# Kernel optimization log

Measured on AMD Instinct MI355X. Metric: run time of the kernel, lower is better.

## Reference

```python
import jax, jax.numpy as jnp
import numpy as np

N_NODES = 100000
N_EDGES = 3200000
F_IN = 16


def gcn_conv(x, edge_index, W, b):
    """PyG GCNConv: x' = D^{-1/2} (A + I) D^{-1/2} (x W) + b,
    with degree computed after adding self-loops."""
    n = x.shape[0]
    xw = x @ W  # [N, F_out]
    row, col = edge_index[0], edge_index[1]  # messages flow row -> col
    ones = jnp.ones(row.shape, dtype=x.dtype)
    deg = jax.ops.segment_sum(ones, col, num_segments=n) + 1.0  # +1 for self-loop
    dinv = jax.lax.rsqrt(deg)  # [N]
    norm = dinv[row] * dinv[col]  # [E]
    msg = xw[row] * norm[:, None]  # [E, F_out]
    out = jax.ops.segment_sum(msg, col, num_segments=n)
    out = out + xw * (1.0 / deg)[:, None]  # self-loop term: norm = 1/deg
    return out + b


def setup_inputs() -> dict:
    key = jax.random.key(0)
    ks = jax.random.split(key, 8)
    x = jax.random.normal(ks[0], (N_NODES, F_IN), dtype=jnp.float32)
    edge_index = jax.random.randint(ks[1], (2, N_EDGES), 0, N_NODES, dtype=jnp.int32)
    # GCNConv weights (glorot in PyG; random normal scaled for the reference)
    W1 = jax.random.normal(ks[2], (F_IN, 4), dtype=jnp.float32) * 0.3
    W2 = jax.random.normal(ks[3], (4, 2), dtype=jnp.float32) * 0.5
    W3 = jax.random.normal(ks[4], (2, 1), dtype=jnp.float32) * 0.7
    b1 = jnp.zeros((4,), jnp.float32)
    b2 = jnp.zeros((2,), jnp.float32)
    b3 = jnp.zeros((1,), jnp.float32)
    return {"x": x, "edge_index": edge_index, "W1": W1, "b1": b1,
            "W2": W2, "b2": b2, "W3": W3, "b3": b3}


def reference(x, edge_index, W1, b1, W2, b2, W3, b3):
    # encode(): GCNConv -> relu -> GCNConv -> relu -> GCNConv -> tanh
    # (dropout is identity in eval mode)
    h = jax.nn.relu(gcn_conv(x, edge_index, W1, b1))
    h = jax.nn.relu(gcn_conv(h, edge_index, W2, b2))
    return jnp.tanh(gcn_conv(h, edge_index, W3, b3))  # [N, 1]
```

## Files before the change

kernel.cpp:

```cpp
#include <hip/hip_runtime.h>
#include <math.h>


static constexpr int BLK    = 256;
static constexpr int BSHIFT = 7;
static constexpr int BCOLS  = 128;
static constexpr int CAP    = 5120;
static constexpr int PAD    = 16;
static constexpr int PBLK   = 512;
static constexpr int PITER  = 25;
static constexpr int SBLK   = 512;
static constexpr int GBLK   = 512;

__global__ void zero_cnt_kernel(int* __restrict__ cnt, int len) {
    int i = blockIdx.x * blockDim.x + threadIdx.x;
    if (i < len) cnt[i] = 0;
}

__global__ __launch_bounds__(PBLK) void partition_kernel(
        const int* __restrict__ row, const int* __restrict__ col,
        int* __restrict__ cnt, unsigned int* __restrict__ part,
        int e, int nbuck) {
    __shared__ int hist[1024];
    for (int j = threadIdx.x; j < nbuck; j += PBLK) hist[j] = 0;
    __syncthreads();

    const int base = blockIdx.x * (PBLK * PITER) + (int)threadIdx.x;
    unsigned int pay[PITER];
    unsigned int meta[PITER];
#pragma unroll
    for (int i = 0; i < PITER; ++i) {
        int idx = base + i * PBLK;
        bool ok = idx < e;
        int c = ok ? col[idx] : 0;
        int r = ok ? row[idx] : 0;
        int bk = c >> BSHIFT;
        pay[i] = ((unsigned int)(c & (BCOLS - 1)) << 17) | (unsigned int)r;
        if (ok) {
            int rnk = atomicAdd(&hist[bk], 1);
            meta[i] = ((unsigned int)bk << 18) | (unsigned int)rnk;
        } else {
            meta[i] = 0xFFFFFFFFu;
        }
    }
    __syncthreads();

    for (int j = threadIdx.x; j < nbuck; j += PBLK) {
        int h = hist[j];
        hist[j] = h ? atomicAdd(&cnt[j * PAD], h) : 0;
    }
    __syncthreads();

#pragma unroll
    for (int i = 0; i < PITER; ++i) {
        if (meta[i] != 0xFFFFFFFFu) {
            int bk  = (int)(meta[i] >> 18);
            int rnk = (int)(meta[i] & 0x3FFFFu);
            int off = hist[bk] + rnk;
            if (off < CAP)
                part[(size_t)bk * CAP + off] = pay[i];
        }
    }
}

__global__ __launch_bounds__(SBLK) void sort_y1_kernel(
        unsigned int* __restrict__ part, const int* __restrict__ cnt,
        const float* __restrict__ x, const float* __restrict__ W1,
        int* __restrict__ rs, int* __restrict__ re, float* __restrict__ dinv,
        float* __restrict__ y1, int n) {
    __shared__ unsigned int staged[CAP];
    __shared__ unsigned short srank[CAP];
    __shared__ int hist[BCOLS];
    __shared__ int scanb[BCOLS];
    const int b = blockIdx.x;
    const int m = min(cnt[b * PAD], CAP);
    const size_t segbase = (size_t)b * CAP;

    if (threadIdx.x < BCOLS) hist[threadIdx.x] = 0;
    __syncthreads();
    for (int k = threadIdx.x; k < m; k += SBLK) {
        unsigned int v = part[segbase + k];
        staged[k] = v;
        srank[k] = (unsigned short)atomicAdd(&hist[v >> 17], 1);
    }
    __syncthreads();

    if (threadIdx.x < BCOLS) scanb[threadIdx.x] = hist[threadIdx.x];
    __syncthreads();
    for (int off = 1; off < BCOLS; off <<= 1) {
        int v = 0;
        if (threadIdx.x < BCOLS && (int)threadIdx.x >= off)
            v = scanb[threadIdx.x - off];
        __syncthreads();
        if (threadIdx.x < BCOLS) scanb[threadIdx.x] += v;
        __syncthreads();
    }

    for (int k = threadIdx.x; k < m; k += SBLK) {
        unsigned int v = staged[k];
        int lc = (int)(v >> 17);
        int pos = (scanb[lc] - hist[lc]) + (int)srank[k];
        part[segbase + pos] = v & 0x1FFFFu;
    }

    int lc = (int)threadIdx.x >> 2;
    int f  = (int)threadIdx.x & 3;
    int node = b * BCOLS + lc;
    if (node < n) {
        int deg = hist[lc];
        float di = rsqrtf((float)(deg + 1));
        if (f == 0) {
            int start = (int)segbase + (scanb[lc] - deg);
            rs[node] = start;
            re[node] = start + deg;
            dinv[node] = di;
        }
        const float4* x4 = (const float4*)x + (size_t)node * 4;
        float4 r0 = x4[0], r1 = x4[1], r2 = x4[2], r3 = x4[3];
        float a = 0.0f;
        a = fmaf(r0.x, W1[0 * 4 + f], a);  a = fmaf(r0.y, W1[1 * 4 + f], a);
        a = fmaf(r0.z, W1[2 * 4 + f], a);  a = fmaf(r0.w, W1[3 * 4 + f], a);
        a = fmaf(r1.x, W1[4 * 4 + f], a);  a = fmaf(r1.y, W1[5 * 4 + f], a);
        a = fmaf(r1.z, W1[6 * 4 + f], a);  a = fmaf(r1.w, W1[7 * 4 + f], a);
        a = fmaf(r2.x, W1[8 * 4 + f], a);  a = fmaf(r2.y, W1[9 * 4 + f], a);
        a = fmaf(r2.z, W1[10 * 4 + f], a); a = fmaf(r2.w, W1[11 * 4 + f], a);
        a = fmaf(r3.x, W1[12 * 4 + f], a); a = fmaf(r3.y, W1[13 * 4 + f], a);
        a = fmaf(r3.z, W1[14 * 4 + f], a); a = fmaf(r3.w, W1[15 * 4 + f], a);
        y1[node * 4 + f] = a * di;
    }
}

template <int F, int FN, int ACT, int SUBW>
__global__ __launch_bounds__(GBLK) void gather_kernel(
        const int* __restrict__ rs, const int* __restrict__ re,
        const unsigned int* __restrict__ csr,
        const float* __restrict__ y, const float* __restrict__ dinv,
        const float* __restrict__ bias, const float* __restrict__ Wn,
        float* __restrict__ outv, int n) {
    int t = blockIdx.x * GBLK + (int)threadIdx.x;
    int node = t / SUBW;
    int lane = t % SUBW;
    if (node >= n) return;
    int s = rs[node], tend = re[node];
    float acc[F];
#pragma unroll
    for (int f = 0; f < F; ++f) acc[f] = 0.0f;
    const float4* y4 = (const float4*)y;
    const float2* y2p = (const float2*)y;
    for (int k = s + lane; k < tend; k += SUBW) {
        int r = (int)csr[k];
        if constexpr (F == 4) {
            float4 a = y4[r];
            acc[0] += a.x; acc[1] += a.y; acc[2] += a.z; acc[3] += a.w;
        } else if constexpr (F == 2) {
            float2 a = y2p[r];
            acc[0] += a.x; acc[1] += a.y;
        } else {
            acc[0] += y[r];
        }
    }
#pragma unroll
    for (int off = SUBW / 2; off > 0; off >>= 1)
#pragma unroll
        for (int f = 0; f < F; ++f) acc[f] += __shfl_xor(acc[f], off);
    if (lane == 0) {
        float di = dinv[node];
        float h[F];
#pragma unroll
        for (int f = 0; f < F; ++f) {
            float z = di * (acc[f] + y[node * F + f]) + bias[f];
            if (ACT == 1) z = fmaxf(z, 0.0f);
            if (ACT == 2) z = tanhf(z);
            h[f] = z;
        }
        if constexpr (FN > 0) {
            float o[FN];
#pragma unroll
            for (int g = 0; g < FN; ++g) o[g] = 0.0f;
#pragma unroll
            for (int f = 0; f < F; ++f)
#pragma unroll
                for (int g = 0; g < FN; ++g)
                    o[g] = fmaf(h[f], Wn[f * FN + g], o[g]);
#pragma unroll
            for (int g = 0; g < FN; ++g) outv[node * FN + g] = o[g] * di;
        } else {
#pragma unroll
            for (int f = 0; f < F; ++f) outv[node * F + f] = h[f];
        }
    }
}

extern "C" void kernel_launch(void* const* d_in, const int* in_sizes, int n_in,
                              void* d_out, int out_size, void* d_ws, size_t ws_size,
                              hipStream_t stream) {
    const float* x  = (const float*)d_in[0];
    const int*   ei = (const int*)d_in[1];
    const float* W1 = (const float*)d_in[2];
    const float* b1 = (const float*)d_in[3];
    const float* W2 = (const float*)d_in[4];
    const float* b2 = (const float*)d_in[5];
    const float* W3 = (const float*)d_in[6];
    const float* b3 = (const float*)d_in[7];
    float* out = (float*)d_out;

    const int n = in_sizes[0] / 16;
    const int e = in_sizes[1] / 2;
    const int* row = ei;
    const int* col = ei + e;

    const int nbuck = (n + BCOLS - 1) / BCOLS;

    size_t off = 0;
    auto take = [&](size_t cnt_) {
        char* p = (char*)d_ws + off * 4;
        off += (cnt_ + 15) & ~(size_t)15;
        return p;
    };
    int* cnt           = (int*)take((size_t)nbuck * PAD);
    unsigned int* part = (unsigned int*)take((size_t)nbuck * CAP);
    int* rs            = (int*)take(n);
    int* re            = (int*)take(n);
    float* dinv        = (float*)take(n);
    float* y1          = (float*)take(4 * n);
    float* y2          = (float*)take(2 * n);
    float* y3          = (float*)take(n);

    zero_cnt_kernel<<<(nbuck * PAD + BLK - 1) / BLK, BLK, 0, stream>>>(cnt, nbuck * PAD);

    const int pnb = (e + PBLK * PITER - 1) / (PBLK * PITER);
    partition_kernel<<<pnb, PBLK, 0, stream>>>(row, col, cnt, part, e, nbuck);

    sort_y1_kernel<<<nbuck, SBLK, 0, stream>>>(part, cnt, x, W1, rs, re, dinv, y1, n);

    constexpr int SUBW = 8;
    const int gg = (n * SUBW + GBLK - 1) / GBLK;

    gather_kernel<4, 2, 1, SUBW><<<gg, GBLK, 0, stream>>>(rs, re, part, y1, dinv, b1, W2, y2, n);
    gather_kernel<2, 1, 1, SUBW><<<gg, GBLK, 0, stream>>>(rs, re, part, y2, dinv, b2, W3, y3, n);
    gather_kernel<1, 0, 2, SUBW><<<gg, GBLK, 0, stream>>>(rs, re, part, y3, dinv, b3, nullptr, out, n);
}
```

Baseline: 121.8 us.

## Stage partition and sort scatters in shared memory for coalesced global writes

The partition kernel now sorts each block's edges by bucket in shared memory (via a block-wide exclusive scan over bucket counts), then writes them out contiguously so runs of edges for the same bucket land in consecutive global addresses. PITER is halved to fit the staging buffers in LDS, doubling the block count. The sort kernel similarly writes the locally sorted segment to an LDS buffer first and then copies it to global memory linearly. The aim is to replace scattered global writes with coalesced ones, at the cost of extra LDS traffic, more barriers, and lower occupancy from larger shared memory use.

New measurement: 113.3 us. 6.9% less time.

```diff
diff --git a/kernel.cpp b/kernel.cpp
--- a/kernel.cpp
+++ b/kernel.cpp
@@ -5,10 +5,12 @@
 static constexpr int BLK    = 256;
 static constexpr int BSHIFT = 7;
 static constexpr int BCOLS  = 128;
+static constexpr int NBMAX  = 1024;
 static constexpr int CAP    = 5120;
 static constexpr int PAD    = 16;
 static constexpr int PBLK   = 512;
-static constexpr int PITER  = 25;
+static constexpr int PITER  = 13;
+static constexpr int PCHUNK = PBLK * PITER;
 static constexpr int SBLK   = 512;
 static constexpr int GBLK   = 512;
 
@@ -21,45 +23,68 @@
         const int* __restrict__ row, const int* __restrict__ col,
         int* __restrict__ cnt, unsigned int* __restrict__ part,
         int e, int nbuck) {
-    __shared__ int hist[1024];
-    for (int j = threadIdx.x; j < nbuck; j += PBLK) hist[j] = 0;
-    __syncthreads();
-
-    const int base = blockIdx.x * (PBLK * PITER) + (int)threadIdx.x;
+    __shared__ unsigned int   staged[PCHUNK];
+    __shared__ unsigned short bkid[PCHUNK];
+    __shared__ int hist[NBMAX];
+    __shared__ int excl[NBMAX];
+    __shared__ int gbase[NBMAX];
+    __shared__ int sh[PBLK];
+    const int t = (int)threadIdx.x;
+    for (int j = t; j < NBMAX; j += PBLK) hist[j] = 0;
+    __syncthreads();
+
+    const int blockstart = blockIdx.x * PCHUNK;
+    const int m = min(PCHUNK, e - blockstart);
+
     unsigned int pay[PITER];
-    unsigned int meta[PITER];
+    int bks[PITER], rnk[PITER];
 #pragma unroll
     for (int i = 0; i < PITER; ++i) {
-        int idx = base + i * PBLK;
-        bool ok = idx < e;
-        int c = ok ? col[idx] : 0;
-        int r = ok ? row[idx] : 0;
-        int bk = c >> BSHIFT;
-        pay[i] = ((unsigned int)(c & (BCOLS - 1)) << 17) | (unsigned int)r;
-        if (ok) {
-            int rnk = atomicAdd(&hist[bk], 1);
-            meta[i] = ((unsigned int)bk << 18) | (unsigned int)rnk;
+        int idx = blockstart + i * PBLK + t;
+        if (idx < e) {
+            int c = col[idx], r = row[idx];
+            bks[i] = c >> BSHIFT;
+            pay[i] = ((unsigned int)(c & (BCOLS - 1)) << 17) | (unsigned int)r;
+            rnk[i] = atomicAdd(&hist[bks[i]], 1);
         } else {
-            meta[i] = 0xFFFFFFFFu;
-        }
-    }
-    __syncthreads();
-
-    for (int j = threadIdx.x; j < nbuck; j += PBLK) {
+            bks[i] = -1;
+        }
+    }
+    __syncthreads();
+
+    int a0 = hist[2 * t], a1 = hist[2 * t + 1];
+    sh[t] = a0 + a1;
+    __syncthreads();
+    for (int off = 1; off < PBLK; off <<= 1) {
+        int v = (t >= off) ? sh[t - off] : 0;
+        __syncthreads();
+        sh[t] += v;
+        __syncthreads();
+    }
+    int pairExcl = sh[t] - (a0 + a1);
+    excl[2 * t]     = pairExcl;
+    excl[2 * t + 1] = pairExcl + a0;
+    for (int j = t; j < nbuck; j += PBLK) {
         int h = hist[j];
-        hist[j] = h ? atomicAdd(&cnt[j * PAD], h) : 0;
+        gbase[j] = h ? atomicAdd(&cnt[j * PAD], h) : 0;
     }
     __syncthreads();
 
 #pragma unroll
     for (int i = 0; i < PITER; ++i) {
-        if (meta[i] != 0xFFFFFFFFu) {
-            int bk  = (int)(meta[i] >> 18);
-            int rnk = (int)(meta[i] & 0x3FFFFu);
-            int off = hist[bk] + rnk;
-            if (off < CAP)
-                part[(size_t)bk * CAP + off] = pay[i];
-        }
+        if (bks[i] >= 0) {
+            int pos = excl[bks[i]] + rnk[i];
+            staged[pos] = pay[i];
+            bkid[pos]   = (unsigned short)bks[i];
+        }
+    }
+    __syncthreads();
+
+    for (int k = t; k < m; k += PBLK) {
+        int bk  = bkid[k];
+        int off2 = gbase[bk] + (k - excl[bk]);
+        if (off2 < CAP)
+            part[(size_t)bk * CAP + off2] = staged[k];
     }
 }
 
@@ -68,7 +93,8 @@
         const float* __restrict__ x, const float* __restrict__ W1,
         int* __restrict__ rs, int* __restrict__ re, float* __restrict__ dinv,
         float* __restrict__ y1, int n) {
-    __shared__ unsigned int staged[CAP];
+    __shared__ unsigned int   staged[CAP];
+    __shared__ unsigned int   sorted[CAP];
     __shared__ unsigned short srank[CAP];
     __shared__ int hist[BCOLS];
     __shared__ int scanb[BCOLS];
@@ -99,9 +125,12 @@
     for (int k = threadIdx.x; k < m; k += SBLK) {
         unsigned int v = staged[k];
         int lc = (int)(v >> 17);
-        int pos = (scanb[lc] - hist[lc]) + (int)srank[k];
-        part[segbase + pos] = v & 0x1FFFFu;
-    }
+        sorted[(scanb[lc] - hist[lc]) + (int)srank[k]] = v & 0x1FFFFu;
+    }
+    __syncthreads();
+
+    for (int k = threadIdx.x; k < m; k += SBLK)
+        part[segbase + k] = sorted[k];
 
     int lc = (int)threadIdx.x >> 2;
     int f  = (int)threadIdx.x & 3;
@@ -228,7 +257,7 @@
 
     zero_cnt_kernel<<<(nbuck * PAD + BLK - 1) / BLK, BLK, 0, stream>>>(cnt, nbuck * PAD);
 
-    const int pnb = (e + PBLK * PITER - 1) / (PBLK * PITER);
+    const int pnb = (e + PCHUNK - 1) / PCHUNK;
     partition_kernel<<<pnb, PBLK, 0, stream>>>(row, col, cnt, part, e, nbuck);
 
     sort_y1_kernel<<<nbuck, SBLK, 0, stream>>>(part, cnt, x, W1, rs, re, dinv, y1, n);
```
